# Kernel tuning notes

Measured on AMD Instinct MI355X. Metric: run time of the kernel, lower is better.

Reference implementation:

```python
import jax, jax.numpy as jnp
import numpy as np

SIGMA = 0.1
B = 1.0
SPATIAL_WEIGHT = 0.5
EPS = 1e-5


def setup_inputs() -> dict:
    key = jax.random.key(0)
    k1, k2 = jax.random.split(key)
    N, C, H, W = 2, 256, 64, 64
    I_features = jax.random.normal(k1, (N, C, H, W), dtype=jnp.float32)
    T_features = jax.random.normal(k2, (N, C, H, W), dtype=jnp.float32)
    return {"I_features": I_features, "T_features": T_features}


def _calc_cx(raw):
    # raw: [N, P_T, H, W]; min + exp-softmax over the target-patch axis (axis=1)
    mn = jnp.min(raw, axis=1, keepdims=True)
    rel = raw / (mn + EPS)
    w = jnp.exp((B - rel) / SIGMA)
    return w / jnp.sum(w, axis=1, keepdims=True)


def reference(I_features, T_features):
    N, C, H, W = I_features.shape
    P = H * W

    # ---- spatial branch: L2 distances on a normalized meshgrid (C=2) ----
    rows = jnp.arange(H, dtype=jnp.float32) / (H + 1)
    cols = jnp.arange(W, dtype=jnp.float32) / (W + 1)
    grid = jnp.stack(jnp.meshgrid(rows, cols, indexing="ij"))  # [2, H, W]
    g = grid.reshape(2, P)                                      # [2, P]
    sq = jnp.sum(g * g, axis=0)                                 # [P]
    d = sq[:, None] + sq[None, :] - 2.0 * (g.T @ g)             # [P_I, P_T]
    d = jnp.clip(d, 0.0)
    raw_sp = d.T.reshape(1, P, H, W)  # [1, P_T, H, W]; identical per sample
    cx_sp = _calc_cx(raw_sp)

    # ---- feature branch: cosine similarity via centered, L2-normed feats ----
    meanT = jnp.mean(T_features, axis=(0, 2, 3), keepdims=True)
    Ic = I_features - meanT
    Tc = T_features - meanT
    In = Ic / jnp.linalg.norm(Ic, axis=1, keepdims=True)
    Tn = Tc / jnp.linalg.norm(Tc, axis=1, keepdims=True)
    Iv = In.reshape(N, C, P)
    Tv = Tn.reshape(N, C, P)
    dot = jnp.einsum("ncq,ncp->nqp", Tv, Iv)  # [N, P_T, P_I]
    raw_feat = ((1.0 - dot) / 2.0).reshape(N, P, H, W)
    cx_feat = _calc_cx(raw_feat)

    # ---- combine, max over I positions, mean over T patches, -log, mean ----
    cx = (1.0 - SPATIAL_WEIGHT) * cx_feat + SPATIAL_WEIGHT * cx_sp  # [N,P,H,W]
    m = jnp.max(cx, axis=(2, 3))  # [N, P]
    m = jnp.mean(m, axis=1)       # [N]
    return jnp.mean(-jnp.log(m))
```

## Files before the change

kernel.cpp:

```cpp
#include <hip/hip_runtime.h>
#include <math.h>

#define PP 4096
#define CC 256
#define NN 2

typedef __attribute__((ext_vector_type(4))) float f32x4;

__device__ __forceinline__ void gld_lds16(const char* g, char* l) {
    __builtin_amdgcn_global_load_lds(
        (const __attribute__((address_space(1))) unsigned int*)g,
        (__attribute__((address_space(3))) unsigned int*)l, 16, 0, 0);
}

__global__ __launch_bounds__(256) void mean_kernel(const float* __restrict__ T,
                                                   float* __restrict__ meanT,
                                                   unsigned* __restrict__ mn_enc,
                                                   float* __restrict__ S,
                                                   float* __restrict__ diagw) {
    int c = blockIdx.x, tid = threadIdx.x;
    float s = 0.f;
    for (int n = 0; n < NN; n++) {
        const float4* Tc = (const float4*)&T[(size_t)(n * CC + c) * PP];
        for (int g = 0; g < 4; g++) {
            float4 v = Tc[tid + g * 256];
            s += (v.x + v.y) + (v.z + v.w);
        }
    }
    __shared__ float red[256];
    red[tid] = s; __syncthreads();
    for (int st = 128; st > 0; st >>= 1) {
        if (tid < st) red[tid] += red[tid + st];
        __syncthreads();
    }
    if (tid == 0) meanT[c] = red[0] * (1.0f / (NN * PP));
    int base = blockIdx.x * 32;
    if (tid < 32) {
        mn_enc[base + tid] = 0xFFFFFFFFu;
        S[base + tid] = 0.f;
        diagw[base + tid] = 0.f;
    }
}

__global__ __launch_bounds__(256) void normalize_kernel(const float* __restrict__ I,
                                                        const float* __restrict__ T,
                                                        const float* __restrict__ meanT,
                                                        char* __restrict__ InT,
                                                        char* __restrict__ TnT) {
    int pc = blockIdx.x * 32;
    int n = blockIdx.y;
    int which = blockIdx.z;
    const float* X = which ? T : I;
    char* Y = which ? TnT : InT;

    __shared__ float tile[CC][36];
    __shared__ float red[32][32];
    __shared__ float invn[32];

    int tid = threadIdx.x;
    int pl4 = tid & 7, c0 = tid >> 3;
    float sq0 = 0.f, sq1 = 0.f, sq2 = 0.f, sq3 = 0.f;
    for (int c = c0; c < CC; c += 32) {
        float m = meanT[c];
        float4 v = *(const float4*)&X[(size_t)(n * CC + c) * PP + pc + pl4 * 4];
        v.x -= m; v.y -= m; v.z -= m; v.w -= m;
        *(float4*)&tile[c][pl4 * 4] = v;
        sq0 += v.x * v.x; sq1 += v.y * v.y; sq2 += v.z * v.z; sq3 += v.w * v.w;
    }
    red[c0][pl4 * 4 + 0] = sq0;
    red[c0][pl4 * 4 + 1] = sq1;
    red[c0][pl4 * 4 + 2] = sq2;
    red[c0][pl4 * 4 + 3] = sq3;
    __syncthreads();
    if (tid < 32) {
        float s = 0.f;
        for (int k = 0; k < 32; k++) s += red[k][tid];
        invn[tid] = 1.0f / sqrtf(s);
    }
    __syncthreads();
    for (int pass = 0; pass < 8; pass++) {
        int r = pass * 4 + (tid >> 6);
        int c4 = (tid & 63) * 4;
        float in = invn[r];
        float v0 = tile[c4 + 0][r] * in;
        float v1 = tile[c4 + 1][r] * in;
        float v2 = tile[c4 + 2][r] * in;
        float v3 = tile[c4 + 3][r] * in;
        int w = __builtin_amdgcn_cvt_pk_fp8_f32(v0, v1, 0, false);
        w = __builtin_amdgcn_cvt_pk_fp8_f32(v2, v3, w, true);
        *(unsigned*)&Y[(size_t)(n * PP + pc + r) * CC + c4] = (unsigned)w;
    }
}

template <int MODE>
__global__ __launch_bounds__(512, 6) void cx_gemm(const char* __restrict__ TnT,
                                                  const char* __restrict__ InT,
                                                  unsigned* __restrict__ mn_enc,
                                                  float* __restrict__ S,
                                                  float* __restrict__ diagw) {
    const int n = blockIdx.z;
    const char* __restrict__ A = TnT + (size_t)n * PP * CC;
    const char* __restrict__ B = InT + (size_t)n * PP * CC;
    const int q0 = blockIdx.y * 128, p0 = blockIdx.x * 128;

    __shared__ __align__(16) char As[128 * 128];
    __shared__ __align__(16) char Bs[128 * 128];
    __shared__ float red[8][64];

    const int tid = threadIdx.x;
    const int l = tid & 63, wv = tid >> 6;
    const int lm = l & 15, quad = l >> 4;
    const int wr = (wv & 3) * 32, wc = (wv >> 2) * 64;

    const int srow = tid >> 3;
    const int gk = ((tid & 7) ^ ((srow >> 1) & 7)) * 16;
    const char* Ag = A + (size_t)(q0 + srow) * CC + gk;
    const char* Bg = B + (size_t)(p0 + srow) * CC + gk;
    char* Al = As + tid * 16;
    char* Bl = Bs + tid * 16;

    f32x4 acc[2][4] = {};

    const int rsw = (lm & 14);

#pragma unroll
    for (int it = 0; it < 2; it++) {
        __syncthreads();
        gld_lds16(Ag + it * 128, Al);
        gld_lds16(Ag + 64 * CC + it * 128, Al + 8192);
        gld_lds16(Bg + it * 128, Bl);
        gld_lds16(Bg + 64 * CC + it * 128, Bl + 8192);
        __syncthreads();

#pragma unroll
        for (int ksub = 0; ksub < 4; ksub++) {
            const int c = ksub * 4 + quad;
            long a[2], b[4];
#pragma unroll
            for (int i = 0; i < 2; i++)
                a[i] = *(const long*)&As[(wr + i * 16 + lm) * 128 + (c ^ rsw) * 8];
#pragma unroll
            for (int j = 0; j < 4; j++)
                b[j] = *(const long*)&Bs[(wc + j * 16 + lm) * 128 + (c ^ rsw) * 8];
#pragma unroll
            for (int i = 0; i < 2; i++)
#pragma unroll
                for (int j = 0; j < 4; j++)
                    acc[i][j] = __builtin_amdgcn_mfma_f32_16x16x32_fp8_fp8(a[i], b[j], acc[i][j], 0, 0, 0);
        }
    }

    if (MODE == 0) {
#pragma unroll
        for (int j = 0; j < 4; j++) {
            float m = 3.4e38f;
#pragma unroll
            for (int i = 0; i < 2; i++)
#pragma unroll
                for (int e = 0; e < 4; e++)
                    m = fminf(m, (1.0f - acc[i][j][e]) * 0.5f);
            m = fminf(m, __shfl_xor(m, 16));
            m = fminf(m, __shfl_xor(m, 32));
            if (quad == 0) red[wv][j * 16 + lm] = m;
        }
        __syncthreads();
        if (tid < 128) {
            int grp = tid >> 6, idx = tid & 63;
            float m = fminf(fminf(red[grp * 4 + 0][idx], red[grp * 4 + 1][idx]),
                            fminf(red[grp * 4 + 2][idx], red[grp * 4 + 3][idx]));
            unsigned u = __float_as_uint(m);
            u = (u & 0x80000000u) ? ~u : (u | 0x80000000u);
            atomicMin(&mn_enc[n * PP + p0 + tid], u);
        }
    } else {
#pragma unroll
        for (int j = 0; j < 4; j++) {
            const int col = p0 + wc + j * 16 + lm;
            unsigned e = mn_enc[n * PP + col];
            unsigned u = (e & 0x80000000u) ? (e & 0x7fffffffu) : ~e;
            float mnv = __uint_as_float(u);
            float inv2 = 14.4269504f / (mnv + 1e-5f);
            float s = 0.f;
#pragma unroll
            for (int i = 0; i < 2; i++)
#pragma unroll
                for (int e2 = 0; e2 < 4; e2++) {
                    float raw = (1.0f - acc[i][j][e2]) * 0.5f;
                    float w = exp2f(fmaf(raw, -inv2, 14.4269504f));
                    s += w;
                    int q = q0 + wr + i * 16 + quad * 4 + e2;
                    if (q == col) diagw[n * PP + q] = w;
                }
            s += __shfl_xor(s, 16);
            s += __shfl_xor(s, 32);
            if (quad == 0) red[wv][j * 16 + lm] = s;
        }
        __syncthreads();
        if (tid < 128) {
            int grp = tid >> 6, idx = tid & 63;
            float s = red[grp * 4 + 0][idx] + red[grp * 4 + 1][idx] +
                      red[grp * 4 + 2][idx] + red[grp * 4 + 3][idx];
            atomicAdd(&S[n * PP + p0 + tid], s);
        }
    }
}

__global__ __launch_bounds__(1024) void finalize_kernel(const float* __restrict__ S,
                                                        const float* __restrict__ diagw,
                                                        float* __restrict__ out) {
    __shared__ float red[1024];
    int tid = threadIdx.x;
    int n = tid >> 9, t = tid & 511;
    const float4* dv = (const float4*)(diagw + n * PP);
    const float4* sv = (const float4*)(S + n * PP);
    float s = 0.f;
#pragma unroll
    for (int g = 0; g < 2; g++) {
        float4 d = dv[t + g * 512];
        float4 v = sv[t + g * 512];
        s += d.x / v.x + d.y / v.y + d.z / v.z + d.w / v.w;
    }
    red[tid] = s; __syncthreads();
    for (int st = 256; st > 0; st >>= 1) {
        if (t < st) red[n * 512 + t] += red[n * 512 + t + st];
        __syncthreads();
    }
    if (tid == 0) {
        float m0 = 0.5f + 0.5f * (red[0] / (float)PP);
        float m1 = 0.5f + 0.5f * (red[512] / (float)PP);
        out[0] = 0.5f * (-logf(m0) - logf(m1));
    }
}

extern "C" void kernel_launch(void* const* d_in, const int* in_sizes, int n_in,
                              void* d_out, int out_size, void* d_ws, size_t ws_size,
                              hipStream_t stream) {
    const float* I = (const float*)d_in[0];
    const float* T = (const float*)d_in[1];
    float* out = (float*)d_out;

    char* ws = (char*)d_ws;
    const size_t SZ_F8 = (size_t)NN * PP * CC;
    char* InT = ws;
    char* TnT = ws + SZ_F8;
    float* meanT = (float*)(ws + 2 * SZ_F8);
    unsigned* mn = (unsigned*)(ws + 2 * SZ_F8 + 32768);
    float* S = (float*)(ws + 2 * SZ_F8 + 2 * 32768);
    float* diagw = (float*)(ws + 2 * SZ_F8 + 3 * 32768);

    mean_kernel<<<CC, 256, 0, stream>>>(T, meanT, mn, S, diagw);
    normalize_kernel<<<dim3(PP / 32, NN, 2), 256, 0, stream>>>(I, T, meanT, InT, TnT);
    cx_gemm<0><<<dim3(PP / 128, PP / 128, NN), 512, 0, stream>>>(TnT, InT, mn, S, diagw);
    cx_gemm<1><<<dim3(PP / 128, PP / 128, NN), 512, 0, stream>>>(TnT, InT, mn, S, diagw);
    finalize_kernel<<<1, 1024, 0, stream>>>(S, diagw, out);
}
```

Baseline: 115.0 us.

## Fuse min and softmax-sum GEMM passes into one per-strip kernel

After: 121.9 us. 1.06x slower.

```diff
diff --git a/kernel.cpp b/kernel.cpp
--- a/kernel.cpp
+++ b/kernel.cpp
@@ -4,6 +4,8 @@
 #define PP 4096
 #define CC 256
 #define NN 2
+#define QS 256
+#define NSTEP (PP / QS)
 
 typedef __attribute__((ext_vector_type(4))) float f32x4;
 
@@ -13,11 +15,10 @@
         (__attribute__((address_space(3))) unsigned int*)l, 16, 0, 0);
 }
 
+
 __global__ __launch_bounds__(256) void mean_kernel(const float* __restrict__ T,
                                                    float* __restrict__ meanT,
-                                                   unsigned* __restrict__ mn_enc,
-                                                   float* __restrict__ S,
-                                                   float* __restrict__ diagw) {
+                                                   float* __restrict__ loss_acc) {
     int c = blockIdx.x, tid = threadIdx.x;
     float s = 0.f;
     for (int n = 0; n < NN; n++) {
@@ -34,12 +35,7 @@
         __syncthreads();
     }
     if (tid == 0) meanT[c] = red[0] * (1.0f / (NN * PP));
-    int base = blockIdx.x * 32;
-    if (tid < 32) {
-        mn_enc[base + tid] = 0xFFFFFFFFu;
-        S[base + tid] = 0.f;
-        diagw[base + tid] = 0.f;
-    }
+    if (blockIdx.x == 0 && tid < NN) loss_acc[tid] = 0.f;
 }
 
 __global__ __launch_bounds__(256) void normalize_kernel(const float* __restrict__ I,
@@ -92,144 +88,159 @@
     }
 }
 
-template <int MODE>
-__global__ __launch_bounds__(512, 6) void cx_gemm(const char* __restrict__ TnT,
-                                                  const char* __restrict__ InT,
-                                                  unsigned* __restrict__ mn_enc,
-                                                  float* __restrict__ S,
-                                                  float* __restrict__ diagw) {
-    const int n = blockIdx.z;
-    const char* __restrict__ A = TnT + (size_t)n * PP * CC;
-    const char* __restrict__ B = InT + (size_t)n * PP * CC;
-    const int q0 = blockIdx.y * 128, p0 = blockIdx.x * 128;
-
-    __shared__ __align__(16) char As[128 * 128];
-    __shared__ __align__(16) char Bs[128 * 128];
-    __shared__ float red[8][64];
+__global__ __launch_bounds__(512) void cx_strip(const char* __restrict__ TnT,
+                                                const char* __restrict__ InT,
+                                                float* __restrict__ loss_acc) {
+    const int strip = blockIdx.x;
+    const int n = blockIdx.y;
+    const int p0 = strip * 32;
+    const char* __restrict__ Ab = TnT + (size_t)n * PP * CC;
+    const char* __restrict__ Bb = InT + (size_t)n * PP * CC + (size_t)p0 * CC;
+
+    __shared__ __align__(16) char As[2][QS * 256];
+    __shared__ __align__(16) char Bs[32 * 256];
+    __shared__ float redw[8][32];
+    __shared__ float inv2s[32];
+    __shared__ float dwl[32];
 
     const int tid = threadIdx.x;
     const int l = tid & 63, wv = tid >> 6;
     const int lm = l & 15, quad = l >> 4;
-    const int wr = (wv & 3) * 32, wc = (wv >> 2) * 64;
-
-    const int srow = tid >> 3;
-    const int gk = ((tid & 7) ^ ((srow >> 1) & 7)) * 16;
-    const char* Ag = A + (size_t)(q0 + srow) * CC + gk;
-    const char* Bg = B + (size_t)(p0 + srow) * CC + gk;
-    char* Al = As + tid * 16;
-    char* Bl = Bs + tid * 16;
-
-    f32x4 acc[2][4] = {};
-
-    const int rsw = (lm & 14);
-
-#pragma unroll
-    for (int it = 0; it < 2; it++) {
+
+    const int srl = tid >> 4;
+    const int sch = ((tid & 15) ^ (srl & 15)) * 16;
+    const char* Asrc = Ab + srl * 256 + sch;
+    char* Alds = (char*)As + tid * 16;
+
+    gld_lds16(Bb + srl * 256 + sch, (char*)Bs + tid * 16);
+
+    long bf[2][8];
+    float cm[2] = {3.4e38f, 3.4e38f};
+    float inv2[2] = {0.f, 0.f};
+    float ss[2] = {0.f, 0.f};
+    const int qd = p0 >> 8;
+    const int wd = (p0 >> 5) & 7;
+
+#pragma unroll 1
+    for (int pass = 0; pass < 2; pass++) {
+#pragma unroll
+        for (int g = 0; g < 8; g++)
+            gld_lds16(Asrc + g * 8192, Alds + g * 8192);
         __syncthreads();
-        gld_lds16(Ag + it * 128, Al);
-        gld_lds16(Ag + 64 * CC + it * 128, Al + 8192);
-        gld_lds16(Bg + it * 128, Bl);
-        gld_lds16(Bg + 64 * CC + it * 128, Bl + 8192);
-        __syncthreads();
-
-#pragma unroll
-        for (int ksub = 0; ksub < 4; ksub++) {
-            const int c = ksub * 4 + quad;
-            long a[2], b[4];
-#pragma unroll
-            for (int i = 0; i < 2; i++)
-                a[i] = *(const long*)&As[(wr + i * 16 + lm) * 128 + (c ^ rsw) * 8];
-#pragma unroll
-            for (int j = 0; j < 4; j++)
-                b[j] = *(const long*)&Bs[(wc + j * 16 + lm) * 128 + (c ^ rsw) * 8];
-#pragma unroll
-            for (int i = 0; i < 2; i++)
-#pragma unroll
-                for (int j = 0; j < 4; j++)
-                    acc[i][j] = __builtin_amdgcn_mfma_f32_16x16x32_fp8_fp8(a[i], b[j], acc[i][j], 0, 0, 0);
-        }
-    }
-
-    if (MODE == 0) {
-#pragma unroll
-        for (int j = 0; j < 4; j++) {
-            float m = 3.4e38f;
-#pragma unroll
-            for (int i = 0; i < 2; i++)
-#pragma unroll
-                for (int e = 0; e < 4; e++)
-                    m = fminf(m, (1.0f - acc[i][j][e]) * 0.5f);
-            m = fminf(m, __shfl_xor(m, 16));
-            m = fminf(m, __shfl_xor(m, 32));
-            if (quad == 0) red[wv][j * 16 + lm] = m;
-        }
-        __syncthreads();
-        if (tid < 128) {
-            int grp = tid >> 6, idx = tid & 63;
-            float m = fminf(fminf(red[grp * 4 + 0][idx], red[grp * 4 + 1][idx]),
-                            fminf(red[grp * 4 + 2][idx], red[grp * 4 + 3][idx]));
-            unsigned u = __float_as_uint(m);
-            u = (u & 0x80000000u) ? ~u : (u | 0x80000000u);
-            atomicMin(&mn_enc[n * PP + p0 + tid], u);
-        }
-    } else {
-#pragma unroll
-        for (int j = 0; j < 4; j++) {
-            const int col = p0 + wc + j * 16 + lm;
-            unsigned e = mn_enc[n * PP + col];
-            unsigned u = (e & 0x80000000u) ? (e & 0x7fffffffu) : ~e;
-            float mnv = __uint_as_float(u);
-            float inv2 = 14.4269504f / (mnv + 1e-5f);
-            float s = 0.f;
-#pragma unroll
-            for (int i = 0; i < 2; i++)
-#pragma unroll
-                for (int e2 = 0; e2 < 4; e2++) {
-                    float raw = (1.0f - acc[i][j][e2]) * 0.5f;
-                    float w = exp2f(fmaf(raw, -inv2, 14.4269504f));
-                    s += w;
-                    int q = q0 + wr + i * 16 + quad * 4 + e2;
-                    if (q == col) diagw[n * PP + q] = w;
+
+        if (pass == 0) {
+#pragma unroll
+            for (int ct = 0; ct < 2; ct++)
+#pragma unroll
+                for (int ks = 0; ks < 8; ks++) {
+                    int g8 = ks * 4 + quad;
+                    int row = ct * 16 + lm;
+                    bf[ct][ks] = *(const long*)&Bs[row * 256 +
+                                  (((g8 >> 1) ^ (row & 15)) * 16) + (g8 & 1) * 8];
                 }
-            s += __shfl_xor(s, 16);
-            s += __shfl_xor(s, 32);
-            if (quad == 0) red[wv][j * 16 + lm] = s;
-        }
-        __syncthreads();
-        if (tid < 128) {
-            int grp = tid >> 6, idx = tid & 63;
-            float s = red[grp * 4 + 0][idx] + red[grp * 4 + 1][idx] +
-                      red[grp * 4 + 2][idx] + red[grp * 4 + 3][idx];
-            atomicAdd(&S[n * PP + p0 + tid], s);
-        }
-    }
-}
-
-__global__ __launch_bounds__(1024) void finalize_kernel(const float* __restrict__ S,
-                                                        const float* __restrict__ diagw,
-                                                        float* __restrict__ out) {
-    __shared__ float red[1024];
-    int tid = threadIdx.x;
-    int n = tid >> 9, t = tid & 511;
-    const float4* dv = (const float4*)(diagw + n * PP);
-    const float4* sv = (const float4*)(S + n * PP);
-    float s = 0.f;
-#pragma unroll
-    for (int g = 0; g < 2; g++) {
-        float4 d = dv[t + g * 512];
-        float4 v = sv[t + g * 512];
-        s += d.x / v.x + d.y / v.y + d.z / v.z + d.w / v.w;
-    }
-    red[tid] = s; __syncthreads();
-    for (int st = 256; st > 0; st >>= 1) {
-        if (t < st) red[n * 512 + t] += red[n * 512 + t + st];
-        __syncthreads();
-    }
-    if (tid == 0) {
-        float m0 = 0.5f + 0.5f * (red[0] / (float)PP);
-        float m1 = 0.5f + 0.5f * (red[512] / (float)PP);
-        out[0] = 0.5f * (-logf(m0) - logf(m1));
-    }
+        }
+
+#pragma unroll 1
+        for (int qs = 0; qs < NSTEP; qs++) {
+            if (qs < NSTEP - 1) {
+                const char* s = Asrc + (size_t)(qs + 1) * 65536;
+                char* d = Alds + ((qs + 1) & 1) * 65536;
+#pragma unroll
+                for (int g = 0; g < 8; g++)
+                    gld_lds16(s + g * 8192, d + g * 8192);
+            }
+
+            const char* Ac = (const char*)As + (qs & 1) * 65536;
+            f32x4 acc[2][2] = {};
+#pragma unroll
+            for (int ks = 0; ks < 8; ks++) {
+                const int off = (((ks * 2 + (quad >> 1)) ^ lm) * 16) + (quad & 1) * 8;
+                long a[2];
+#pragma unroll
+                for (int i = 0; i < 2; i++)
+                    a[i] = *(const long*)&Ac[(wv * 32 + i * 16 + lm) * 256 + off];
+#pragma unroll
+                for (int i = 0; i < 2; i++)
+#pragma unroll
+                    for (int ct = 0; ct < 2; ct++)
+                        acc[i][ct] = __builtin_amdgcn_mfma_f32_16x16x32_fp8_fp8(
+                            a[i], bf[ct][ks], acc[i][ct], 0, 0, 0);
+            }
+            if (pass == 0) {
+#pragma unroll
+                for (int ct = 0; ct < 2; ct++)
+#pragma unroll
+                    for (int i = 0; i < 2; i++)
+#pragma unroll
+                        for (int e = 0; e < 4; e++)
+                            cm[ct] = fminf(cm[ct], (1.0f - acc[i][ct][e]) * 0.5f);
+            } else {
+                const bool dstep = (qs == qd) && (wv == wd);
+#pragma unroll
+                for (int ct = 0; ct < 2; ct++) {
+                    float s2 = 0.f;
+#pragma unroll
+                    for (int i = 0; i < 2; i++)
+#pragma unroll
+                        for (int e = 0; e < 4; e++) {
+                            float raw = (1.0f - acc[i][ct][e]) * 0.5f;
+                            float w = exp2f(fmaf(raw, -inv2[ct], 14.4269504f));
+                            s2 += w;
+                            if (dstep && (i * 16 + quad * 4 + e == ct * 16 + lm))
+                                dwl[ct * 16 + lm] = w;
+                        }
+                    ss[ct] += s2;
+                }
+            }
+            __syncthreads();
+        }
+
+        if (pass == 0) {
+#pragma unroll
+            for (int ct = 0; ct < 2; ct++) {
+                cm[ct] = fminf(cm[ct], __shfl_xor(cm[ct], 16));
+                cm[ct] = fminf(cm[ct], __shfl_xor(cm[ct], 32));
+                if (quad == 0) redw[wv][ct * 16 + lm] = cm[ct];
+            }
+            __syncthreads();
+            if (tid < 32) {
+                float m = redw[0][tid];
+#pragma unroll
+                for (int w2 = 1; w2 < 8; w2++) m = fminf(m, redw[w2][tid]);
+                inv2s[tid] = 14.4269504f / (m + 1e-5f);
+            }
+            __syncthreads();
+            inv2[0] = inv2s[lm];
+            inv2[1] = inv2s[16 + lm];
+        }
+    }
+
+#pragma unroll
+    for (int ct = 0; ct < 2; ct++) {
+        ss[ct] += __shfl_xor(ss[ct], 16);
+        ss[ct] += __shfl_xor(ss[ct], 32);
+        if (quad == 0) redw[wv][ct * 16 + lm] = ss[ct];
+    }
+    __syncthreads();
+    if (tid < 32) {
+        float s = 0.f;
+#pragma unroll
+        for (int w2 = 0; w2 < 8; w2++) s += redw[w2][tid];
+        float part = dwl[tid] / s;
+        part += __shfl_xor(part, 1);
+        part += __shfl_xor(part, 2);
+        part += __shfl_xor(part, 4);
+        part += __shfl_xor(part, 8);
+        part += __shfl_xor(part, 16);
+        if (tid == 0) atomicAdd(&loss_acc[n], part);
+    }
+}
+
+__global__ void finalize_kernel(const float* __restrict__ loss_acc,
+                                float* __restrict__ out) {
+    float m0 = 0.5f + 0.5f * (loss_acc[0] / (float)PP);
+    float m1 = 0.5f + 0.5f * (loss_acc[1] / (float)PP);
+    out[0] = 0.5f * (-logf(m0) - logf(m1));
 }
 
 extern "C" void kernel_launch(void* const* d_in, const int* in_sizes, int n_in,
@@ -244,13 +255,10 @@
     char* InT = ws;
     char* TnT = ws + SZ_F8;
     float* meanT = (float*)(ws + 2 * SZ_F8);
-    unsigned* mn = (unsigned*)(ws + 2 * SZ_F8 + 32768);
-    float* S = (float*)(ws + 2 * SZ_F8 + 2 * 32768);
-    float* diagw = (float*)(ws + 2 * SZ_F8 + 3 * 32768);
-
-    mean_kernel<<<CC, 256, 0, stream>>>(T, meanT, mn, S, diagw);
+    float* loss_acc = (float*)(ws + 2 * SZ_F8 + 32768);
+
+    mean_kernel<<<CC, 256, 0, stream>>>(T, meanT, loss_acc);
     normalize_kernel<<<dim3(PP / 32, NN, 2), 256, 0, stream>>>(I, T, meanT, InT, TnT);
-    cx_gemm<0><<<dim3(PP / 128, PP / 128, NN), 512, 0, stream>>>(TnT, InT, mn, S, diagw);
-    cx_gemm<1><<<dim3(PP / 128, PP / 128, NN), 512, 0, stream>>>(TnT, InT, mn, S, diagw);
-    finalize_kernel<<<1, 1024, 0, stream>>>(S, diagw, out);
-}
+    cx_strip<<<dim3(PP / 32, NN), 512, 0, stream>>>(TnT, InT, loss_acc);
+    finalize_kernel<<<1, 1, 0, stream>>>(loss_acc, out);
+}
```
